# Optimization experiments

Measured on AMD Instinct MI355X. Metric: run time of the kernel, lower is better.

The kernel has to match this reference:

```python
import jax, jax.numpy as jnp
import numpy as np

THR = 0.2          # config['thr']
BORDER_RM = 2      # config['border_rm']
TEMP = 0.1         # config['dsmax_temperature']


def setup_inputs() -> dict:
    key = jax.random.key(0)
    k0, k1 = jax.random.split(key)
    N, C = 2, 256
    h0c, w0c, h1c, w1c = 60, 80, 60, 80
    return {
        "feat_c0": jax.random.normal(k0, (N, h0c * w0c, C), dtype=jnp.float32),
        "feat_c1": jax.random.normal(k1, (N, h1c * w1c, C), dtype=jnp.float32),
        "h0c": h0c, "w0c": w0c, "h1c": h1c, "w1c": w1c,
    }


def _valid_1d(n: int, b: int):
    # True in the interior [b, n-b), False on the border — matches mask_border writes
    return jnp.zeros((n,), dtype=bool).at[b:n - b].set(True)


def reference(feat_c0, feat_c1, h0c, w0c, h1c, w1c):
    N, L, C = feat_c0.shape
    S = feat_c1.shape[1]
    scale = 1.0 / (C ** 0.5)
    f0 = feat_c0 * scale
    f1 = feat_c1 * scale

    # similarity + dual softmax  -> conf_matrix [N, L, S]
    sim = jnp.einsum('nlc,nsc->nls', f0, f1) / TEMP
    conf = jax.nn.softmax(sim, axis=1) * jax.nn.softmax(sim, axis=2)

    # threshold + border removal (mask_border, vectorized as an interior mask)
    mask = conf > THR
    b = BORDER_RM
    border = (_valid_1d(h0c, b)[:, None, None, None]
              & _valid_1d(w0c, b)[None, :, None, None]
              & _valid_1d(h1c, b)[None, None, :, None]
              & _valid_1d(w1c, b)[None, None, None, :])  # [h0c,w0c,h1c,w1c]
    mask = (mask.reshape(N, h0c, w0c, h1c, w1c) & border[None]).reshape(N, L, S)

    # mutual nearest neighbor
    mask = mask \
        & (conf == conf.max(axis=2, keepdims=True)) \
        & (conf == conf.max(axis=1, keepdims=True))

    # match extraction, expressed densely (static shapes for jit):
    # mask_v[b,i] = row i of pair b has a match; j_ids its column; mconf its confidence
    mask_v = mask.any(axis=2)                               # [N, L]
    j_ids = jnp.argmax(mask, axis=2)                        # [N, L] (first True)
    mconf = jnp.take_along_axis(conf, j_ids[:, :, None], axis=2)[..., 0]
    mconf = jnp.where(mask_v, mconf, 0.0)                   # [N, L]

    # coarse keypoint coords for matched columns: (x, y) = (j % w1c, j // w1c)
    mkpts1_c = jnp.stack([j_ids % w1c, j_ids // w1c], axis=-1)  # [N, L, 2]

    return conf, mask_v, j_ids, mkpts1_c, mconf
```

## Files before the change

### kernel.cpp

```cpp
#include <hip/hip_runtime.h>

typedef _Float16 half8 __attribute__((ext_vector_type(8)));
typedef float f32x4 __attribute__((ext_vector_type(4)));

#define NB 2
#define LS 4800
#define CCH 256
#define W0 80
#define W1 80
#define THRV 0.2f
#define SQS 0.19764235376052370f

#define TN 38
#define PADL 4864

#define OF_RM   0
#define OF_RSI  9600
#define OF_CM   19200
#define OF_CSI  28800
#define OF_RWM  38400
#define OF_CAND 48000
#define OF_CLM  57600
#define OF_PROW 67200
#define OF_PCOL (67200 + 739328)
#define OF_AH   (67200 + 2*739328)
#define OF_BH   (OF_AH + 1228800)

#define O_MASKV 46080000ull
#define O_JIDS  46089600ull
#define O_MKPT  46099200ull
#define O_MCONF 46118400ull

__device__ __forceinline__ void load_lds16(const void* g, void* l) {
    __builtin_amdgcn_global_load_lds((const __attribute__((address_space(1))) void*)g,
                                     (__attribute__((address_space(3))) void*)l, 16, 0, 0);
}

__global__ __launch_bounds__(256) void conv_half(const float* __restrict__ A,
                                                 const float* __restrict__ B,
                                                 float* __restrict__ ws) {
    const int which = blockIdx.y;
    const float* src = which ? B : A;
    _Float16* dst = (_Float16*)(ws + (which ? OF_BH : OF_AH));
    const int idx = blockIdx.x * 256 + threadIdx.x;
    const float4 v = ((const float4*)src)[idx];
    union { _Float16 h[4]; uint2 u; } p;
    p.h[0] = (_Float16)(v.x * SQS);
    p.h[1] = (_Float16)(v.y * SQS);
    p.h[2] = (_Float16)(v.z * SQS);
    p.h[3] = (_Float16)(v.w * SQS);
    ((uint2*)dst)[idx] = p.u;
}

__global__ __launch_bounds__(256, 2) void gemm_mfma(float* __restrict__ out,
                                                    float* __restrict__ ws) {
    __shared__ __align__(16) union {
        struct { _Float16 A[8192]; _Float16 B[8192]; } st;
        struct { float rs[128][2][2]; float cs[128][2][2]; } red;
    } sm;
    const int bx = blockIdx.x, by = blockIdx.y, n = blockIdx.z;
    const _Float16* Ah = (const _Float16*)(ws + OF_AH) + (size_t)n * LS * CCH;
    const _Float16* Bh = (const _Float16*)(ws + OF_BH) + (size_t)n * LS * CCH;
    const int tid = threadIdx.x;
    const int lane = tid & 63, w = tid >> 6;
    const int wx = w & 1, wy = w >> 1;
    const int m = lane & 15, quad = lane >> 4;

    f32x4 acc[4][4];
    {
        f32x4 z = {0.f, 0.f, 0.f, 0.f};
#pragma unroll
        for (int a = 0; a < 4; a++)
#pragma unroll
            for (int b = 0; b < 4; b++) acc[a][b] = z;
    }

    const int srow = lane >> 3;
    const int qst = (lane & 7) ^ (srow & 7);

    for (int kt = 0; kt < 4; kt++) {
        const int k0 = kt * 64;
#pragma unroll
        for (int i = 0; i < 4; i++) {
            const int c = i * 4 + w;
            int gr = by * 128 + c * 8 + srow; gr = gr < LS ? gr : LS - 1;
            load_lds16(Ah + (size_t)gr * CCH + k0 + qst * 8, &sm.st.A[c * 512]);
        }
#pragma unroll
        for (int i = 0; i < 4; i++) {
            const int c = i * 4 + w;
            int gr = bx * 128 + c * 8 + srow; gr = gr < LS ? gr : LS - 1;
            load_lds16(Bh + (size_t)gr * CCH + k0 + qst * 8, &sm.st.B[c * 512]);
        }
        __syncthreads();
#pragma unroll
        for (int t = 0; t < 2; t++) {
            half8 Af[4], Bf[4];
#pragma unroll
            for (int a = 0; a < 4; a++) {
                const int rl = wy * 64 + a * 16 + m;
                const int sl = rl * 8 + ((t * 4 + quad) ^ (rl & 7));
                Af[a] = *(const half8*)&sm.st.A[sl * 8];
            }
#pragma unroll
            for (int b = 0; b < 4; b++) {
                const int cl = wx * 64 + b * 16 + m;
                const int sl = cl * 8 + ((t * 4 + quad) ^ (cl & 7));
                Bf[b] = *(const half8*)&sm.st.B[sl * 8];
            }
#pragma unroll
            for (int a = 0; a < 4; a++)
#pragma unroll
                for (int b = 0; b < 4; b++)
                    acc[a][b] = __builtin_amdgcn_mfma_f32_16x16x32_f16(Af[a], Bf[b], acc[a][b], 0, 0, 0);
        }
        __syncthreads();
    }

    const int l0 = by * 128, s0 = bx * 128;
    float* On = out + (size_t)n * LS * LS;
#pragma unroll
    for (int a = 0; a < 4; a++) {
        const int gr0 = l0 + wy * 64 + a * 16 + quad * 4;
#pragma unroll
        for (int reg = 0; reg < 4; reg++) {
            const int gr = gr0 + reg;
            if (gr < LS) {
#pragma unroll
                for (int b = 0; b < 4; b++) {
                    const int gc = s0 + wx * 64 + b * 16 + m;
                    if (gc < LS) On[(size_t)gr * LS + gc] = acc[a][b][reg];
                }
            }
        }
    }

    bool bval[4];
#pragma unroll
    for (int b = 0; b < 4; b++) bval[b] = (s0 + wx * 64 + b * 16 + m) < LS;
    bool aval[4][4];
#pragma unroll
    for (int a = 0; a < 4; a++)
#pragma unroll
        for (int reg = 0; reg < 4; reg++)
            aval[a][reg] = (l0 + wy * 64 + a * 16 + quad * 4 + reg) < LS;

#pragma unroll
    for (int a = 0; a < 4; a++) {
#pragma unroll
        for (int reg = 0; reg < 4; reg++) {
            float mx = -1e30f;
#pragma unroll
            for (int b = 0; b < 4; b++) if (bval[b]) mx = fmaxf(mx, acc[a][b][reg]);
            for (int d = 1; d < 16; d <<= 1) mx = fmaxf(mx, __shfl_xor(mx, d, 64));
            float sum = 0.f;
#pragma unroll
            for (int b = 0; b < 4; b++) if (bval[b]) sum += __expf(acc[a][b][reg] - mx);
            for (int d = 1; d < 16; d <<= 1) sum += __shfl_xor(sum, d, 64);
            if (m == 0) {
                const int rl = wy * 64 + a * 16 + quad * 4 + reg;
                sm.red.rs[rl][wx][0] = mx; sm.red.rs[rl][wx][1] = sum;
            }
        }
    }
#pragma unroll
    for (int b = 0; b < 4; b++) {
        float mx = -1e30f;
#pragma unroll
        for (int a = 0; a < 4; a++)
#pragma unroll
            for (int reg = 0; reg < 4; reg++)
                if (aval[a][reg]) mx = fmaxf(mx, acc[a][b][reg]);
        float sum = 0.f;
#pragma unroll
        for (int a = 0; a < 4; a++)
#pragma unroll
            for (int reg = 0; reg < 4; reg++)
                if (aval[a][reg]) sum += __expf(acc[a][b][reg] - mx);
        for (int d = 16; d < 64; d <<= 1) {
            const float mo = __shfl_xor(mx, d, 64);
            const float so = __shfl_xor(sum, d, 64);
            const float nm = fmaxf(mx, mo);
            sum = sum * __expf(mx - nm) + so * __expf(mo - nm);
            mx = nm;
        }
        if (quad == 0) {
            const int cl = wx * 64 + b * 16 + m;
            sm.red.cs[cl][wy][0] = mx; sm.red.cs[cl][wy][1] = sum;
        }
    }
    __syncthreads();
    if (tid < 128) {
        const float m0 = sm.red.rs[tid][0][0], v0 = sm.red.rs[tid][0][1];
        const float m1 = sm.red.rs[tid][1][0], v1 = sm.red.rs[tid][1][1];
        const float nm = fmaxf(m0, m1);
        const float s = v0 * __expf(m0 - nm) + v1 * __expf(m1 - nm);
        ((float2*)(ws + OF_PROW))[((size_t)n * TN + bx) * PADL + by * 128 + tid] = make_float2(nm, s);
    } else {
        const int t = tid - 128;
        const float m0 = sm.red.cs[t][0][0], v0 = sm.red.cs[t][0][1];
        const float m1 = sm.red.cs[t][1][0], v1 = sm.red.cs[t][1][1];
        const float nm = fmaxf(m0, m1);
        const float s = v0 * __expf(m0 - nm) + v1 * __expf(m1 - nm);
        ((float2*)(ws + OF_PCOL))[((size_t)n * TN + by) * PADL + bx * 128 + t] = make_float2(nm, s);
    }
}

__global__ __launch_bounds__(256) void combine_stats(float* __restrict__ ws) {
    const int idx = blockIdx.x * 256 + threadIdx.x;
    const int half_ = idx >= 9600;
    const int i = idx - half_ * 9600;
    const int n = i / LS, r = i % LS;
    const float2* P = (const float2*)(ws + (half_ ? OF_PCOL : OF_PROW)) + (size_t)n * TN * PADL + r;
    float M = -1e30f, S = 0.f;
    for (int b = 0; b < TN; b++) {
        const float2 p = P[(size_t)b * PADL];
        const float nm = fmaxf(M, p.x);
        S = S * __expf(M - nm) + p.y * __expf(p.x - nm);
        M = nm;
    }
    if (!half_) {
        ws[OF_RM + i] = M; ws[OF_RSI + i] = 1.0f / S;
        ws[OF_CLM + i] = 0.0f;
    } else {
        ws[OF_CM + i] = M; ws[OF_CSI + i] = 1.0f / S;
    }
}

__global__ __launch_bounds__(256) void conf_pass(float* __restrict__ conf,
                                                 float* __restrict__ ws) {
    const int chunk = blockIdx.x, n = blockIdx.y;
    const int tid = threadIdx.x;
    const int r0 = chunk * 16;
    __shared__ float Lv[16][256];
    __shared__ int Li[16][256];
    __shared__ float Mv[16][16];
    __shared__ int Mi[16][16];
    float cmv[19], csiv[19], cmax[19];
#pragma unroll
    for (int j = 0; j < 19; j++) {
        const int s = tid + j * 256;
        cmax[j] = 0.f;
        if (s < LS) { cmv[j] = ws[OF_CM + n * LS + s]; csiv[j] = ws[OF_CSI + n * LS + s]; }
        else { cmv[j] = 0.f; csiv[j] = 0.f; }
    }
    for (int r = 0; r < 16; r++) {
        const int gr = r0 + r;
        const float rm = ws[OF_RM + n * LS + gr];
        const float rsi = ws[OF_RSI + n * LS + gr];
        float* row = conf + ((size_t)n * LS + gr) * LS;
        float lmax = -1.f; int lidx = 0;
#pragma unroll
        for (int j = 0; j < 19; j++) {
            const int s = tid + j * 256;
            if (s < LS) {
                const float x = row[s];
                const float c = __expf(2.f * x - rm - cmv[j]) * (rsi * csiv[j]);
                row[s] = c;
                cmax[j] = fmaxf(cmax[j], c);
                if (c > lmax) { lmax = c; lidx = s; }
            }
        }
        Lv[r][tid] = lmax; Li[r][tid] = lidx;
    }
    __syncthreads();
    {
        const int r = tid >> 4, p = tid & 15;
        float bv = -2.f; int bi = 0;
        for (int k = 0; k < 16; k++) {
            const float v = Lv[r][p * 16 + k]; const int ii = Li[r][p * 16 + k];
            if (v > bv || (v == bv && ii < bi)) { bv = v; bi = ii; }
        }
        Mv[r][p] = bv; Mi[r][p] = bi;
    }
    __syncthreads();
    if (tid < 16) {
        float bv = -2.f; int bi = 0;
        for (int p = 0; p < 16; p++) {
            const float v = Mv[tid][p]; const int ii = Mi[tid][p];
            if (v > bv || (v == bv && ii < bi)) { bv = v; bi = ii; }
        }
        ws[OF_RWM + n * LS + r0 + tid] = bv;
        ((int*)ws)[OF_CAND + n * LS + r0 + tid] = bi;
    }
    int* clm = (int*)ws + OF_CLM + n * LS;
#pragma unroll
    for (int j = 0; j < 19; j++) {
        const int s = tid + j * 256;
        if (s < LS && cmax[j] > 0.f) atomicMax(&clm[s], __float_as_int(cmax[j]));
    }
}

__global__ __launch_bounds__(256) void match_pass(const float* __restrict__ ws,
                                                  float* __restrict__ out) {
    const int idx = blockIdx.x * 256 + threadIdx.x;
    if (idx >= NB * LS) return;
    const int n = idx / LS, l = idx % LS;
    const float rwm = ws[OF_RWM + idx];
    const int cand = ((const int*)ws)[OF_CAND + idx];
    const float clm = ws[OF_CLM + n * LS + cand];
    const int y0 = l / W0, x0 = l % W0;
    const int y1 = cand / W1, x1 = cand % W1;
    const bool b0 = (y0 >= 2 && y0 < 58 && x0 >= 2 && x0 < 78);
    const bool b1 = (y1 >= 2 && y1 < 58 && x1 >= 2 && x1 < 78);
    const bool matched = (rwm > THRV) && b0 && b1 && (rwm == clm);
    const int j = matched ? cand : 0;
    out[O_MASKV + idx] = matched ? 1.f : 0.f;
    out[O_JIDS + idx] = (float)j;
    out[O_MKPT + (size_t)idx * 2 + 0] = (float)(j % W1);
    out[O_MKPT + (size_t)idx * 2 + 1] = (float)(j / W1);
    out[O_MCONF + idx] = matched ? rwm : 0.f;
}

extern "C" void kernel_launch(void* const* d_in, const int* in_sizes, int n_in,
                              void* d_out, int out_size, void* d_ws, size_t ws_size,
                              hipStream_t stream) {
    const float* f0 = (const float*)d_in[0];
    const float* f1 = (const float*)d_in[1];
    float* out = (float*)d_out;
    float* ws = (float*)d_ws;

    conv_half<<<dim3(2400, 2), 256, 0, stream>>>(f0, f1, ws);
    gemm_mfma<<<dim3(TN, TN, NB), 256, 0, stream>>>(out, ws);
    combine_stats<<<75, 256, 0, stream>>>(ws);
    conf_pass<<<dim3(300, NB), 256, 0, stream>>>(out, ws);
    match_pass<<<38, 256, 0, stream>>>(ws, out);
}
```

Before: 328.8 us.

## Recompute GEMM in a second pass to fuse conf write and max reductions

The old pipeline wrote raw logits to the 184MB output and read them back in a separate conf pass. The new one runs the GEMM twice. The first pass only produces softmax statistics, using one tile-wide max as the shift. The second pass recomputes the logits and writes the final confidence directly, with per-tile row argmax and column max partials that a new combine kernel reduces, replacing the atomics. This trades a duplicated GEMM (K=256) for removing one full write and one full read of the large matrix. The tile-wide max shift also risks exp underflow when logits within a tile have a large spread.

```diff
diff --git a/kernel.cpp b/kernel.cpp
--- a/kernel.cpp
+++ b/kernel.cpp
@@ -14,10 +14,8 @@
 #define TN 38
 #define PADL 4864
 
-#define OF_RM   0
-#define OF_RSI  9600
-#define OF_CM   19200
-#define OF_CSI  28800
+#define OF_RST  0
+#define OF_CST  19200
 #define OF_RWM  38400
 #define OF_CAND 48000
 #define OF_CLM  57600
@@ -52,8 +50,58 @@
     ((uint2*)dst)[idx] = p.u;
 }
 
-__global__ __launch_bounds__(256, 2) void gemm_mfma(float* __restrict__ out,
-                                                    float* __restrict__ ws) {
+__device__ __forceinline__ void gemm_core(const _Float16* __restrict__ Ah,
+                                          const _Float16* __restrict__ Bh,
+                                          _Float16* smA, _Float16* smB,
+                                          const int bx, const int by,
+                                          const int tid, f32x4 (&acc)[4][4]) {
+    const int lane = tid & 63, w = tid >> 6;
+    const int wx = w & 1, wy = w >> 1;
+    const int m = lane & 15, quad = lane >> 4;
+    const int srow = lane >> 3;
+    const int qst = (lane & 7) ^ (srow & 7);
+
+    for (int kt = 0; kt < 4; kt++) {
+        const int k0 = kt * 64;
+#pragma unroll
+        for (int i = 0; i < 4; i++) {
+            const int c = i * 4 + w;
+            int gr = by * 128 + c * 8 + srow; gr = gr < LS ? gr : LS - 1;
+            load_lds16(Ah + (size_t)gr * CCH + k0 + qst * 8, &smA[c * 512]);
+        }
+#pragma unroll
+        for (int i = 0; i < 4; i++) {
+            const int c = i * 4 + w;
+            int gr = bx * 128 + c * 8 + srow; gr = gr < LS ? gr : LS - 1;
+            load_lds16(Bh + (size_t)gr * CCH + k0 + qst * 8, &smB[c * 512]);
+        }
+        __syncthreads();
+#pragma unroll
+        for (int t = 0; t < 2; t++) {
+            half8 Af[4], Bf[4];
+#pragma unroll
+            for (int a = 0; a < 4; a++) {
+                const int rl = wy * 64 + a * 16 + m;
+                const int sl = rl * 8 + ((t * 4 + quad) ^ (rl & 7));
+                Af[a] = *(const half8*)&smA[sl * 8];
+            }
+#pragma unroll
+            for (int b = 0; b < 4; b++) {
+                const int cl = wx * 64 + b * 16 + m;
+                const int sl = cl * 8 + ((t * 4 + quad) ^ (cl & 7));
+                Bf[b] = *(const half8*)&smB[sl * 8];
+            }
+#pragma unroll
+            for (int a = 0; a < 4; a++)
+#pragma unroll
+                for (int b = 0; b < 4; b++)
+                    acc[a][b] = __builtin_amdgcn_mfma_f32_16x16x32_f16(Af[a], Bf[b], acc[a][b], 0, 0, 0);
+        }
+        __syncthreads();
+    }
+}
+
+__global__ __launch_bounds__(256, 2) void gemm_stats(float* __restrict__ ws) {
     __shared__ __align__(16) union {
         struct { _Float16 A[8192]; _Float16 B[8192]; } st;
         struct { float rs[128][2][2]; float cs[128][2][2]; } red;
@@ -74,119 +122,61 @@
 #pragma unroll
             for (int b = 0; b < 4; b++) acc[a][b] = z;
     }
-
-    const int srow = lane >> 3;
-    const int qst = (lane & 7) ^ (srow & 7);
-
-    for (int kt = 0; kt < 4; kt++) {
-        const int k0 = kt * 64;
-#pragma unroll
-        for (int i = 0; i < 4; i++) {
-            const int c = i * 4 + w;
-            int gr = by * 128 + c * 8 + srow; gr = gr < LS ? gr : LS - 1;
-            load_lds16(Ah + (size_t)gr * CCH + k0 + qst * 8, &sm.st.A[c * 512]);
-        }
-#pragma unroll
-        for (int i = 0; i < 4; i++) {
-            const int c = i * 4 + w;
-            int gr = bx * 128 + c * 8 + srow; gr = gr < LS ? gr : LS - 1;
-            load_lds16(Bh + (size_t)gr * CCH + k0 + qst * 8, &sm.st.B[c * 512]);
-        }
-        __syncthreads();
-#pragma unroll
-        for (int t = 0; t < 2; t++) {
-            half8 Af[4], Bf[4];
-#pragma unroll
-            for (int a = 0; a < 4; a++) {
-                const int rl = wy * 64 + a * 16 + m;
-                const int sl = rl * 8 + ((t * 4 + quad) ^ (rl & 7));
-                Af[a] = *(const half8*)&sm.st.A[sl * 8];
-            }
-#pragma unroll
-            for (int b = 0; b < 4; b++) {
-                const int cl = wx * 64 + b * 16 + m;
-                const int sl = cl * 8 + ((t * 4 + quad) ^ (cl & 7));
-                Bf[b] = *(const half8*)&sm.st.B[sl * 8];
-            }
-#pragma unroll
-            for (int a = 0; a < 4; a++)
+    gemm_core(Ah, Bh, sm.st.A, sm.st.B, bx, by, tid, acc);
+
+    const int l0 = by * 128, s0 = bx * 128;
+    bool bval[4];
+#pragma unroll
+    for (int b = 0; b < 4; b++) bval[b] = (s0 + wx * 64 + b * 16 + m) < LS;
+
+    float T = -1e30f;
+#pragma unroll
+    for (int a = 0; a < 4; a++)
+#pragma unroll
+        for (int reg = 0; reg < 4; reg++) {
+            if ((l0 + wy * 64 + a * 16 + quad * 4 + reg) < LS) {
 #pragma unroll
                 for (int b = 0; b < 4; b++)
-                    acc[a][b] = __builtin_amdgcn_mfma_f32_16x16x32_f16(Af[a], Bf[b], acc[a][b], 0, 0, 0);
-        }
-        __syncthreads();
-    }
-
-    const int l0 = by * 128, s0 = bx * 128;
-    float* On = out + (size_t)n * LS * LS;
-#pragma unroll
-    for (int a = 0; a < 4; a++) {
-        const int gr0 = l0 + wy * 64 + a * 16 + quad * 4;
+                    if (bval[b]) T = fmaxf(T, acc[a][b][reg]);
+            }
+        }
+#pragma unroll
+    for (int d = 1; d < 64; d <<= 1) T = fmaxf(T, __shfl_xor(T, d, 64));
+
+#pragma unroll
+    for (int a = 0; a < 4; a++)
 #pragma unroll
         for (int reg = 0; reg < 4; reg++) {
-            const int gr = gr0 + reg;
-            if (gr < LS) {
-#pragma unroll
-                for (int b = 0; b < 4; b++) {
-                    const int gc = s0 + wx * 64 + b * 16 + m;
-                    if (gc < LS) On[(size_t)gr * LS + gc] = acc[a][b][reg];
-                }
-            }
-        }
-    }
-
-    bool bval[4];
-#pragma unroll
-    for (int b = 0; b < 4; b++) bval[b] = (s0 + wx * 64 + b * 16 + m) < LS;
-    bool aval[4][4];
+            const bool rv = (l0 + wy * 64 + a * 16 + quad * 4 + reg) < LS;
+#pragma unroll
+            for (int b = 0; b < 4; b++)
+                acc[a][b][reg] = (rv && bval[b]) ? __expf(acc[a][b][reg] - T) : 0.f;
+        }
+
 #pragma unroll
     for (int a = 0; a < 4; a++)
 #pragma unroll
-        for (int reg = 0; reg < 4; reg++)
-            aval[a][reg] = (l0 + wy * 64 + a * 16 + quad * 4 + reg) < LS;
-
-#pragma unroll
-    for (int a = 0; a < 4; a++) {
-#pragma unroll
         for (int reg = 0; reg < 4; reg++) {
-            float mx = -1e30f;
-#pragma unroll
-            for (int b = 0; b < 4; b++) if (bval[b]) mx = fmaxf(mx, acc[a][b][reg]);
-            for (int d = 1; d < 16; d <<= 1) mx = fmaxf(mx, __shfl_xor(mx, d, 64));
-            float sum = 0.f;
-#pragma unroll
-            for (int b = 0; b < 4; b++) if (bval[b]) sum += __expf(acc[a][b][reg] - mx);
-            for (int d = 1; d < 16; d <<= 1) sum += __shfl_xor(sum, d, 64);
+            float s = acc[a][0][reg] + acc[a][1][reg] + acc[a][2][reg] + acc[a][3][reg];
+#pragma unroll
+            for (int d = 1; d < 16; d <<= 1) s += __shfl_xor(s, d, 64);
             if (m == 0) {
                 const int rl = wy * 64 + a * 16 + quad * 4 + reg;
-                sm.red.rs[rl][wx][0] = mx; sm.red.rs[rl][wx][1] = sum;
-            }
-        }
-    }
+                sm.red.rs[rl][wx][0] = T; sm.red.rs[rl][wx][1] = s;
+            }
+        }
 #pragma unroll
     for (int b = 0; b < 4; b++) {
-        float mx = -1e30f;
+        float s = 0.f;
 #pragma unroll
         for (int a = 0; a < 4; a++)
 #pragma unroll
-            for (int reg = 0; reg < 4; reg++)
-                if (aval[a][reg]) mx = fmaxf(mx, acc[a][b][reg]);
-        float sum = 0.f;
-#pragma unroll
-        for (int a = 0; a < 4; a++)
-#pragma unroll
-            for (int reg = 0; reg < 4; reg++)
-                if (aval[a][reg]) sum += __expf(acc[a][b][reg] - mx);
-        for (int d = 16; d < 64; d <<= 1) {
-            const float mo = __shfl_xor(mx, d, 64);
-            const float so = __shfl_xor(sum, d, 64);
-            const float nm = fmaxf(mx, mo);
-            sum = sum * __expf(mx - nm) + so * __expf(mo - nm);
-            mx = nm;
-        }
+            for (int reg = 0; reg < 4; reg++) s += acc[a][b][reg];
+        s += __shfl_xor(s, 16, 64);
+        s += __shfl_xor(s, 32, 64);
         if (quad == 0) {
             const int cl = wx * 64 + b * 16 + m;
-            sm.red.cs[cl][wy][0] = mx; sm.red.cs[cl][wy][1] = sum;
+            sm.red.cs[cl][wy][0] = T; sm.red.cs[cl][wy][1] = s;
         }
     }
     __syncthreads();
@@ -219,75 +209,129 @@
         S = S * __expf(M - nm) + p.y * __expf(p.x - nm);
         M = nm;
     }
+    ((float2*)(ws + (half_ ? OF_CST : OF_RST)))[n * LS + r] = make_float2(M, 1.0f / S);
+}
+
+__global__ __launch_bounds__(256, 2) void gemm_conf(float* __restrict__ out,
+                                                    float* __restrict__ ws) {
+    __shared__ __align__(16) union {
+        struct { _Float16 A[8192]; _Float16 B[8192]; } st;
+        struct { float rst[128][2]; float cst[128][2];
+                 float rsv[128][2][2]; float csv[128][2]; } ep;
+    } sm;
+    const int bx = blockIdx.x, by = blockIdx.y, n = blockIdx.z;
+    const _Float16* Ah = (const _Float16*)(ws + OF_AH) + (size_t)n * LS * CCH;
+    const _Float16* Bh = (const _Float16*)(ws + OF_BH) + (size_t)n * LS * CCH;
+    const int tid = threadIdx.x;
+    const int lane = tid & 63, w = tid >> 6;
+    const int wx = w & 1, wy = w >> 1;
+    const int m = lane & 15, quad = lane >> 4;
+
+    f32x4 acc[4][4];
+    {
+        f32x4 z = {0.f, 0.f, 0.f, 0.f};
+#pragma unroll
+        for (int a = 0; a < 4; a++)
+#pragma unroll
+            for (int b = 0; b < 4; b++) acc[a][b] = z;
+    }
+    gemm_core(Ah, Bh, sm.st.A, sm.st.B, bx, by, tid, acc);
+
+    const int l0 = by * 128, s0 = bx * 128;
+    if (tid < 128) {
+        int r = l0 + tid; r = r < LS ? r : LS - 1;
+        const float2 v = ((const float2*)(ws + OF_RST))[n * LS + r];
+        sm.ep.rst[tid][0] = v.x; sm.ep.rst[tid][1] = v.y;
+    } else {
+        const int t = tid - 128;
+        int c = s0 + t; c = c < LS ? c : LS - 1;
+        const float2 v = ((const float2*)(ws + OF_CST))[n * LS + c];
+        sm.ep.cst[t][0] = v.x; sm.ep.cst[t][1] = v.y;
+    }
+    __syncthreads();
+
+    float* On = out + (size_t)n * LS * LS;
+    float colm[4] = {-1.f, -1.f, -1.f, -1.f};
+    bool bval[4]; int gc4[4]; float cmx[4], csi[4];
+#pragma unroll
+    for (int b = 0; b < 4; b++) {
+        const int cl = wx * 64 + b * 16 + m;
+        gc4[b] = s0 + cl;
+        bval[b] = gc4[b] < LS;
+        cmx[b] = sm.ep.cst[cl][0]; csi[b] = sm.ep.cst[cl][1];
+    }
+#pragma unroll
+    for (int a = 0; a < 4; a++) {
+#pragma unroll
+        for (int reg = 0; reg < 4; reg++) {
+            const int rl = wy * 64 + a * 16 + quad * 4 + reg;
+            const int gr = l0 + rl;
+            const float rm = sm.ep.rst[rl][0], rsi = sm.ep.rst[rl][1];
+            const bool rv = gr < LS;
+            float bestv = -1.f; int besti = 0;
+#pragma unroll
+            for (int b = 0; b < 4; b++) {
+                const float c = __expf(2.f * acc[a][b][reg] - rm - cmx[b]) * (rsi * csi[b]);
+                if (rv && bval[b]) {
+                    On[(size_t)gr * LS + gc4[b]] = c;
+                    if (c > bestv) { bestv = c; besti = gc4[b]; }
+                    colm[b] = fmaxf(colm[b], c);
+                }
+            }
+#pragma unroll
+            for (int d = 1; d < 16; d <<= 1) {
+                const float ov = __shfl_xor(bestv, d, 64);
+                const int oi = __shfl_xor(besti, d, 64);
+                if (ov > bestv || (ov == bestv && oi < besti)) { bestv = ov; besti = oi; }
+            }
+            if (m == 0) {
+                sm.ep.rsv[rl][wx][0] = bestv;
+                sm.ep.rsv[rl][wx][1] = __int_as_float(besti);
+            }
+        }
+    }
+#pragma unroll
+    for (int b = 0; b < 4; b++) {
+        float v = colm[b];
+        v = fmaxf(v, __shfl_xor(v, 16, 64));
+        v = fmaxf(v, __shfl_xor(v, 32, 64));
+        if (quad == 0) sm.ep.csv[wx * 64 + b * 16 + m][wy] = v;
+    }
+    __syncthreads();
+    if (tid < 128) {
+        const float v0 = sm.ep.rsv[tid][0][0]; const int i0 = __float_as_int(sm.ep.rsv[tid][0][1]);
+        const float v1 = sm.ep.rsv[tid][1][0]; const int i1 = __float_as_int(sm.ep.rsv[tid][1][1]);
+        float bv; int bi;
+        if (v0 > v1 || (v0 == v1 && i0 <= i1)) { bv = v0; bi = i0; } else { bv = v1; bi = i1; }
+        ((float2*)(ws + OF_PROW))[((size_t)n * TN + bx) * PADL + by * 128 + tid] =
+            make_float2(bv, __int_as_float(bi));
+    } else {
+        const int t = tid - 128;
+        const float v = fmaxf(sm.ep.csv[t][0], sm.ep.csv[t][1]);
+        (ws + OF_PCOL)[((size_t)n * TN + by) * PADL + bx * 128 + t] = v;
+    }
+}
+
+__global__ __launch_bounds__(256) void combine_max(float* __restrict__ ws) {
+    const int idx = blockIdx.x * 256 + threadIdx.x;
+    const int half_ = idx >= 9600;
+    const int i = idx - half_ * 9600;
+    const int n = i / LS, r = i % LS;
     if (!half_) {
-        ws[OF_RM + i] = M; ws[OF_RSI + i] = 1.0f / S;
-        ws[OF_CLM + i] = 0.0f;
+        const float2* P = (const float2*)(ws + OF_PROW) + (size_t)n * TN * PADL + r;
+        float bv = -2.f; int bi = 0;
+        for (int b = 0; b < TN; b++) {
+            const float2 p = P[(size_t)b * PADL];
+            const int pi = __float_as_int(p.y);
+            if (p.x > bv || (p.x == bv && pi < bi)) { bv = p.x; bi = pi; }
+        }
+        ws[OF_RWM + i] = bv;
+        ((int*)ws)[OF_CAND + i] = bi;
     } else {
-        ws[OF_CM + i] = M; ws[OF_CSI + i] = 1.0f / S;
-    }
-}
-
-__global__ __launch_bounds__(256) void conf_pass(float* __restrict__ conf,
-                                                 float* __restrict__ ws) {
-    const int chunk = blockIdx.x, n = blockIdx.y;
-    const int tid = threadIdx.x;
-    const int r0 = chunk * 16;
-    __shared__ float Lv[16][256];
-    __shared__ int Li[16][256];
-    __shared__ float Mv[16][16];
-    __shared__ int Mi[16][16];
-    float cmv[19], csiv[19], cmax[19];
-#pragma unroll
-    for (int j = 0; j < 19; j++) {
-        const int s = tid + j * 256;
-        cmax[j] = 0.f;
-        if (s < LS) { cmv[j] = ws[OF_CM + n * LS + s]; csiv[j] = ws[OF_CSI + n * LS + s]; }
-        else { cmv[j] = 0.f; csiv[j] = 0.f; }
-    }
-    for (int r = 0; r < 16; r++) {
-        const int gr = r0 + r;
-        const float rm = ws[OF_RM + n * LS + gr];
-        const float rsi = ws[OF_RSI + n * LS + gr];
-        float* row = conf + ((size_t)n * LS + gr) * LS;
-        float lmax = -1.f; int lidx = 0;
-#pragma unroll
-        for (int j = 0; j < 19; j++) {
-            const int s = tid + j * 256;
-            if (s < LS) {
-                const float x = row[s];
-                const float c = __expf(2.f * x - rm - cmv[j]) * (rsi * csiv[j]);
-                row[s] = c;
-                cmax[j] = fmaxf(cmax[j], c);
-                if (c > lmax) { lmax = c; lidx = s; }
-            }
-        }
-        Lv[r][tid] = lmax; Li[r][tid] = lidx;
-    }
-    __syncthreads();
-    {
-        const int r = tid >> 4, p = tid & 15;
-        float bv = -2.f; int bi = 0;
-        for (int k = 0; k < 16; k++) {
-            const float v = Lv[r][p * 16 + k]; const int ii = Li[r][p * 16 + k];
-            if (v > bv || (v == bv && ii < bi)) { bv = v; bi = ii; }
-        }
-        Mv[r][p] = bv; Mi[r][p] = bi;
-    }
-    __syncthreads();
-    if (tid < 16) {
-        float bv = -2.f; int bi = 0;
-        for (int p = 0; p < 16; p++) {
-            const float v = Mv[tid][p]; const int ii = Mi[tid][p];
-            if (v > bv || (v == bv && ii < bi)) { bv = v; bi = ii; }
-        }
-        ws[OF_RWM + n * LS + r0 + tid] = bv;
-        ((int*)ws)[OF_CAND + n * LS + r0 + tid] = bi;
-    }
-    int* clm = (int*)ws + OF_CLM + n * LS;
-#pragma unroll
-    for (int j = 0; j < 19; j++) {
-        const int s = tid + j * 256;
-        if (s < LS && cmax[j] > 0.f) atomicMax(&clm[s], __float_as_int(cmax[j]));
+        const float* P = ws + OF_PCOL + (size_t)n * TN * PADL + r;
+        float v = -2.f;
+        for (int b = 0; b < TN; b++) v = fmaxf(v, P[(size_t)b * PADL]);
+        ws[OF_CLM + i] = v;
     }
 }
 
@@ -321,8 +365,9 @@
     float* ws = (float*)d_ws;
 
     conv_half<<<dim3(2400, 2), 256, 0, stream>>>(f0, f1, ws);
-    gemm_mfma<<<dim3(TN, TN, NB), 256, 0, stream>>>(out, ws);
+    gemm_stats<<<dim3(TN, TN, NB), 256, 0, stream>>>(ws);
     combine_stats<<<75, 256, 0, stream>>>(ws);
-    conf_pass<<<dim3(300, NB), 256, 0, stream>>>(out, ws);
+    gemm_conf<<<dim3(TN, TN, NB), 256, 0, stream>>>(out, ws);
+    combine_max<<<75, 256, 0, stream>>>(ws);
     match_pass<<<38, 256, 0, stream>>>(ws, out);
 }
```

New measurement: 306.8 us. -6.7%, faster.
